# Optimization experiments

Hardware: AMD Instinct MI355X
Metric: run time of the kernel (lower is better)

The kernel has to match this reference:

```python
import jax
jax.config.update("jax_enable_x64", True)  # hashing needs true int64 like torch
import jax.numpy as jnp
import numpy as np
import itertools

N_DIM = 3
N_ENTRIES = 4194304  # 2**22
N_FEATURE = 4
BATCH = 2097152  # 2**21 sample points
GRIDS = np.array([128.0, 128.0, 128.0], dtype=np.float32)
PRIMES = np.array([1, 19349663, 83492791], dtype=np.int64)
BIT_TABLE = np.array(list(itertools.product([0, 1], repeat=N_DIM)), dtype=np.int32)  # (2^D, D)


def setup_inputs() -> dict:
    key = jax.random.key(0)
    k1, k2 = jax.random.split(key)
    position = jax.random.uniform(k1, (BATCH, N_DIM), dtype=jnp.float32)  # in [0,1)^D
    hash_table = (jax.random.uniform(k2, (N_ENTRIES, N_FEATURE), dtype=jnp.float32) - 0.5) * 2e-4
    return {"position": position, "hash_table": hash_table}


def reference(position, hash_table):
    grids = jnp.asarray(GRIDS)           # (D,) float32
    bit = jnp.asarray(BIT_TABLE)         # (2^D, D) int32
    primes = jnp.asarray(PRIMES)         # (D,) int64

    # findGrid: lower corner on the integer grid
    lower = jnp.floor(position * grids).astype(jnp.int32)          # (B, D)
    # all 2^D corners of the enclosing cell
    corner = lower[:, None, :] + bit[None, :, :]                    # (B, 2^D, D)

    # spatial hash: XOR of index*prime, reduced mod table size each step (as torch does)
    h = jnp.zeros(corner.shape[:-1], dtype=jnp.int64)               # (B, 2^D)
    for i in range(N_DIM):
        h = jnp.bitwise_xor(h, corner[..., i].astype(jnp.int64) * primes[i]) % N_ENTRIES

    corner_value = hash_table[h]                                    # (B, 2^D, F) gather

    # multilinear interpolation coefficients (faithful to source's weight assignment)
    lower_f = lower / grids                                         # (B, D)
    upper_f = (lower + 1) / grids                                   # (B, D)
    size = (upper_f - lower_f)[0]                                   # (D,) uniform cell size
    coef = jnp.stack([(position - lower_f) / size,
                      (upper_f - position) / size], axis=-1)        # (B, D, 2)
    # weight per corner = prod over dims of the bit-selected coefficient
    w = jnp.prod(coef[:, jnp.arange(N_DIM)[None, :], bit], axis=2)  # (B, 2^D)

    return jnp.sum(corner_value * w[..., None], axis=1)             # (B, F)
```

## Files before the change

### kernel.cpp

```cpp
#include <hip/hip_runtime.h>
#include <stdint.h>


#define HASH_MASK 0x3FFFFFu
#define P1 19349663u
#define P2 83492791u
#define NBUCK 64
#define CHUNKS 16
#define FB 64
#define NSUP 4096
#define PPT 16
#define K3_BLOCK 256
#define PPB (K3_BLOCK * PPT)
#define CMAX 2560

__device__ __forceinline__ uint32_t bucket_of(float px, float py, float pz) {
    uint32_t bx = ((uint32_t)(int)floorf(px * 128.0f)) >> 5;
    uint32_t by = ((uint32_t)(int)floorf(py * 128.0f)) >> 5;
    uint32_t bz = ((uint32_t)(int)floorf(pz * 128.0f)) >> 5;
    return (bx << 4) | (by << 2) | bz;
}

__device__ __forceinline__ uint32_t fine_of(float px, float py, float pz) {
    uint32_t fx = (((uint32_t)(int)floorf(px * 128.0f)) >> 3) & 3u;
    uint32_t fy = (((uint32_t)(int)floorf(py * 128.0f)) >> 3) & 3u;
    uint32_t fz = (((uint32_t)(int)floorf(pz * 128.0f)) >> 3) & 3u;
    return (fx << 4) | (fy << 2) | fz;
}

__device__ __forceinline__ float4 interp_point(float px, float py, float pz,
                                               const float* __restrict__ table) {
    int lx = (int)floorf(px * 128.0f);
    int ly = (int)floorf(py * 128.0f);
    int lz = (int)floorf(pz * 128.0f);
    const float inv = 1.0f / 128.0f;
    float w0x = (px - (float)lx * inv) * 128.0f;
    float w1x = ((float)(lx + 1) * inv - px) * 128.0f;
    float w0y = (py - (float)ly * inv) * 128.0f;
    float w1y = ((float)(ly + 1) * inv - py) * 128.0f;
    float w0z = (pz - (float)lz * inv) * 128.0f;
    float w1z = ((float)(lz + 1) * inv - pz) * 128.0f;
    uint32_t hx0 = (uint32_t)lx, hx1 = (uint32_t)(lx + 1);
    uint32_t hy0 = (uint32_t)ly * P1, hy1 = (uint32_t)(ly + 1) * P1;
    uint32_t hz0 = (uint32_t)lz * P2, hz1 = (uint32_t)(lz + 1) * P2;
    float acc0 = 0.f, acc1 = 0.f, acc2 = 0.f, acc3 = 0.f;
#pragma unroll
    for (int c = 0; c < 8; ++c) {
        int bx = (c >> 2) & 1, by = (c >> 1) & 1, bz = c & 1;
        uint32_t h = ((bx ? hx1 : hx0) ^ (by ? hy1 : hy0) ^ (bz ? hz1 : hz0)) & HASH_MASK;
        const float4 v = *reinterpret_cast<const float4*>(table + (size_t)h * 4);
        float w = ((bx ? w1x : w0x) * (by ? w1y : w0y)) * (bz ? w1z : w0z);
        acc0 += v.x * w; acc1 += v.y * w; acc2 += v.z * w; acc3 += v.w * w;
    }
    return make_float4(acc0, acc1, acc2, acc3);
}

__global__ __launch_bounds__(K3_BLOCK) void hist_kernel(
    const float* __restrict__ pos, uint32_t* __restrict__ hist, int batch)
{
    __shared__ uint32_t h[NBUCK];
    int tid = threadIdx.x;
    size_t start = (size_t)blockIdx.x * PPB;
    if (tid < NBUCK) h[tid] = 0;
    __syncthreads();
#pragma unroll
    for (int k = 0; k < PPT; ++k) {
        size_t i = start + (size_t)k * K3_BLOCK + tid;
        if (i < (size_t)batch) {
            float px = pos[3 * i + 0];
            float py = pos[3 * i + 1];
            float pz = pos[3 * i + 2];
            atomicAdd(&h[bucket_of(px, py, pz)], 1u);
        }
    }
    __syncthreads();
    if (tid < NBUCK && h[tid]) atomicAdd(&hist[tid], h[tid]);
}

__global__ __launch_bounds__(64) void scan_kernel(
    const uint32_t* __restrict__ hist, uint32_t* __restrict__ cursor)
{
    int t = threadIdx.x;
    uint32_t v = hist[t];
    uint32_t inc = v;
    for (int off = 1; off < 64; off <<= 1) {
        uint32_t n = __shfl_up(inc, off);
        if (t >= off) inc += n;
    }
    cursor[t] = inc - v;
}

__global__ __launch_bounds__(K3_BLOCK) void scatter_kernel(
    const float* __restrict__ pos, uint32_t* __restrict__ cursor,
    float4* __restrict__ sorted, int batch)
{
    __shared__ float4 staged[PPB];
    __shared__ uint32_t h[NBUCK], lbase[NBUCK], gbase[NBUCK], lcur[NBUCK];
    int tid = threadIdx.x;
    size_t start = (size_t)blockIdx.x * PPB;

    if (tid < NBUCK) h[tid] = 0;
    __syncthreads();

    float px[PPT], py[PPT], pz[PPT];
    uint32_t bb[PPT];
#pragma unroll
    for (int k = 0; k < PPT; ++k) {
        size_t i = start + (size_t)k * K3_BLOCK + tid;
        px[k] = pos[3 * i + 0];
        py[k] = pos[3 * i + 1];
        pz[k] = pos[3 * i + 2];
        bb[k] = bucket_of(px[k], py[k], pz[k]);
        atomicAdd(&h[bb[k]], 1u);
    }
    __syncthreads();

    if (tid < NBUCK) {
        uint32_t v = h[tid];
        uint32_t inc = v;
        for (int off = 1; off < 64; off <<= 1) {
            uint32_t n = __shfl_up(inc, off);
            if (tid >= off) inc += n;
        }
        uint32_t excl = inc - v;
        lbase[tid] = excl;
        lcur[tid] = excl;
        gbase[tid] = atomicAdd(&cursor[tid], v);
    }
    __syncthreads();

#pragma unroll
    for (int k = 0; k < PPT; ++k) {
        size_t i = start + (size_t)k * K3_BLOCK + tid;
        uint32_t slot = atomicAdd(&lcur[bb[k]], 1u);
        staged[slot] = make_float4(px[k], py[k], pz[k], __uint_as_float((uint32_t)i));
    }
    __syncthreads();

#pragma unroll
    for (int k = 0; k < PPT; ++k) {
        int j = k * K3_BLOCK + tid;
        float4 s = staged[j];
        uint32_t b = bucket_of(s.x, s.y, s.z);
        sorted[gbase[b] + ((uint32_t)j - lbase[b])] = s;
    }
}

__global__ __launch_bounds__(256) void fineA_kernel(
    const float4* __restrict__ sorted, const uint32_t* __restrict__ cursor,
    uint32_t* __restrict__ chist)
{
    __shared__ uint32_t h[FB];
    int tid = threadIdx.x;
    int b = blockIdx.x >> 4, c = blockIdx.x & (CHUNKS - 1);
    uint32_t bs = b ? cursor[b - 1] : 0u;
    uint32_t be = cursor[b];
    uint32_t n = be - bs;
    uint32_t csz = (n + CHUNKS - 1) / CHUNKS;
    uint32_t cs = bs + (uint32_t)c * csz;
    uint32_t ce = min(cs + csz, be);

    if (tid < FB) h[tid] = 0;
    __syncthreads();
    for (uint32_t j = cs + tid; j < ce; j += 256) {
        float4 s = sorted[j];
        atomicAdd(&h[fine_of(s.x, s.y, s.z)], 1u);
    }
    __syncthreads();
    if (tid < FB) chist[((uint32_t)blockIdx.x << 6) + tid] = h[tid];
}

__global__ __launch_bounds__(64) void fineB_kernel(
    uint32_t* __restrict__ chist, const uint32_t* __restrict__ cursor,
    uint32_t* __restrict__ sstart)
{
    int b = blockIdx.x;
    int f = threadIdx.x;
    uint32_t bs = b ? cursor[b - 1] : 0u;

    uint32_t cnt[CHUNKS];
    uint32_t tot = 0;
#pragma unroll
    for (int c = 0; c < CHUNKS; ++c) {
        cnt[c] = chist[(((uint32_t)b * CHUNKS + c) << 6) + f];
        tot += cnt[c];
    }
    uint32_t inc = tot;
    for (int off = 1; off < 64; off <<= 1) {
        uint32_t n = __shfl_up(inc, off);
        if (f >= off) inc += n;
    }
    uint32_t fbase = bs + inc - tot;
    sstart[((uint32_t)b << 6) + f] = fbase;
    uint32_t run = fbase;
#pragma unroll
    for (int c = 0; c < CHUNKS; ++c) {
        chist[(((uint32_t)b * CHUNKS + c) << 6) + f] = run;
        run += cnt[c];
    }
}

__global__ __launch_bounds__(256) void fineC_kernel(
    const float4* __restrict__ sorted, const uint32_t* __restrict__ cursor,
    const uint32_t* __restrict__ cbase, float4* __restrict__ sorted2)
{
    __shared__ float4 staged[CMAX];
    __shared__ uint32_t h[FB], lbase[FB], lcur[FB], gb[FB];
    int tid = threadIdx.x;
    int b = blockIdx.x >> 4, c = blockIdx.x & (CHUNKS - 1);
    uint32_t bs = b ? cursor[b - 1] : 0u;
    uint32_t be = cursor[b];
    uint32_t n = be - bs;
    uint32_t csz = (n + CHUNKS - 1) / CHUNKS;
    uint32_t cs = bs + (uint32_t)c * csz;
    uint32_t ce = min(cs + csz, be);
    if (ce <= cs) return;
    uint32_t m = ce - cs;

    if (tid < FB) h[tid] = 0;
    __syncthreads();

    for (uint32_t j = cs + tid; j < ce; j += 256)  {
        float4 s = sorted[j];
        atomicAdd(&h[fine_of(s.x, s.y, s.z)], 1u);
    }
    __syncthreads();

    if (tid < FB) {
        uint32_t v = h[tid];
        uint32_t inc = v;
        for (int off = 1; off < 64; off <<= 1) {
            uint32_t nn = __shfl_up(inc, off);
            if (tid >= off) inc += nn;
        }
        lbase[tid] = inc - v;
        lcur[tid] = inc - v;
        gb[tid] = cbase[(((uint32_t)b * CHUNKS + c) << 6) + tid];
    }
    __syncthreads();

    for (uint32_t j = cs + tid; j < ce; j += 256) {
        float4 s = sorted[j];
        uint32_t slot = atomicAdd(&lcur[fine_of(s.x, s.y, s.z)], 1u);
        staged[slot] = s;
    }
    __syncthreads();

    for (uint32_t j = tid; j < m; j += 256) {
        float4 s = staged[j];
        uint32_t f = fine_of(s.x, s.y, s.z);
        sorted2[gb[f] + (j - lbase[f])] = s;
    }
}

__global__ __launch_bounds__(256) void interp_super_kernel(
    const float4* __restrict__ sorted2, const uint32_t* __restrict__ sstart,
    const float* __restrict__ table, float4* __restrict__ out4, int batch)
{
    __shared__ float4 corners[729];
    int bid = blockIdx.x;
    int swz = (bid & 7) * (NSUP >> 3) + (bid >> 3);
    int tid = threadIdx.x;
    uint32_t r = (uint32_t)swz;
    uint32_t start = sstart[r];
    uint32_t end = (r == NSUP - 1) ? (uint32_t)batch : sstart[r + 1];
    if (start >= end) return;

    float4 s0 = sorted2[start];
    int rbx = (((int)floorf(s0.x * 128.0f)) >> 3) << 3;
    int rby = (((int)floorf(s0.y * 128.0f)) >> 3) << 3;
    int rbz = (((int)floorf(s0.z * 128.0f)) >> 3) << 3;

    for (int idx = tid; idx < 729; idx += 256) {
        int ci = idx / 81;
        int rem = idx - ci * 81;
        int cj = rem / 9;
        int ck = rem - cj * 9;
        uint32_t h = ((uint32_t)(rbx + ci) ^
                      (uint32_t)(rby + cj) * P1 ^
                      (uint32_t)(rbz + ck) * P2) & HASH_MASK;
        corners[idx] = *reinterpret_cast<const float4*>(table + (size_t)h * 4);
    }
    __syncthreads();

    const float inv = 1.0f / 128.0f;
    for (uint32_t p = start + tid; p < end; p += 256) {
        float4 s = sorted2[p];
        float px = s.x, py = s.y, pz = s.z;
        int lx = (int)floorf(px * 128.0f);
        int ly = (int)floorf(py * 128.0f);
        int lz = (int)floorf(pz * 128.0f);
        float w0x = (px - (float)lx * inv) * 128.0f;
        float w1x = ((float)(lx + 1) * inv - px) * 128.0f;
        float w0y = (py - (float)ly * inv) * 128.0f;
        float w1y = ((float)(ly + 1) * inv - py) * 128.0f;
        float w0z = (pz - (float)lz * inv) * 128.0f;
        float w1z = ((float)(lz + 1) * inv - pz) * 128.0f;
        int li = lx - rbx, lj = ly - rby, lk = lz - rbz;
        int base = li * 81 + lj * 9 + lk;

        float acc0 = 0.f, acc1 = 0.f, acc2 = 0.f, acc3 = 0.f;
#pragma unroll
        for (int c = 0; c < 8; ++c) {
            int bx = (c >> 2) & 1, by = (c >> 1) & 1, bz = c & 1;
            float4 v = corners[base + bx * 81 + by * 9 + bz];
            float w = ((bx ? w1x : w0x) * (by ? w1y : w0y)) * (bz ? w1z : w0z);
            acc0 += v.x * w; acc1 += v.y * w; acc2 += v.z * w; acc3 += v.w * w;
        }
        out4[__float_as_uint(s.w)] = make_float4(acc0, acc1, acc2, acc3);
    }
}

__global__ __launch_bounds__(256) void interp_scatter_kernel(
    const float4* __restrict__ sorted, const float* __restrict__ table,
    float4* __restrict__ out4, int batch, int nwg)
{
    int bid = blockIdx.x;
    int q = nwg >> 3;
    int swz = (bid & 7) * q + (bid >> 3);
    int i = swz * 256 + threadIdx.x;
    if (i >= batch) return;
    float4 s = sorted[i];
    float4 r = interp_point(s.x, s.y, s.z, table);
    out4[__float_as_uint(s.w)] = r;
}

__global__ __launch_bounds__(256) void interp_direct_kernel(
    const float* __restrict__ pos, const float* __restrict__ table,
    float4* __restrict__ out4, int batch)
{
    int i = blockIdx.x * 256 + threadIdx.x;
    if (i >= batch) return;
    out4[i] = interp_point(pos[3 * (size_t)i], pos[3 * (size_t)i + 1],
                           pos[3 * (size_t)i + 2], table);
}

extern "C" void kernel_launch(void* const* d_in, const int* in_sizes, int n_in,
                              void* d_out, int out_size, void* d_ws, size_t ws_size,
                              hipStream_t stream) {
    const float* pos   = (const float*)d_in[0];
    const float* table = (const float*)d_in[1];
    float4* out4 = (float4*)d_out;

    int batch = in_sizes[0] / 3;
    int blocks256 = (batch + 255) / 256;

    size_t sorted_off  = 512;
    size_t sorted2_off = sorted_off + (size_t)batch * 16;
    size_t chist_off   = sorted2_off + (size_t)batch * 16;
    size_t chist_bytes = (size_t)NBUCK * CHUNKS * FB * 4;
    size_t sstart_off  = chist_off + chist_bytes;
    size_t need_min  = sorted_off + (size_t)batch * 16;
    size_t need_full = sstart_off + (size_t)NSUP * 4;

    bool exact = (batch % PPB == 0) && ((blocks256 & 7) == 0);
    if (ws_size < need_min || !exact) {
        interp_direct_kernel<<<blocks256, 256, 0, stream>>>(pos, table, out4, batch);
        return;
    }

    uint32_t* hist    = (uint32_t*)d_ws;
    uint32_t* cursor  = (uint32_t*)((char*)d_ws + 256);
    float4*   sorted  = (float4*)((char*)d_ws + sorted_off);
    float4*   sorted2 = (float4*)((char*)d_ws + sorted2_off);
    uint32_t* chist   = (uint32_t*)((char*)d_ws + chist_off);
    uint32_t* sstart  = (uint32_t*)((char*)d_ws + sstart_off);

    int sblocks = batch / PPB;

    hipMemsetAsync(hist, 0, NBUCK * sizeof(uint32_t), stream);
    hist_kernel<<<sblocks, K3_BLOCK, 0, stream>>>(pos, hist, batch);
    scan_kernel<<<1, 64, 0, stream>>>(hist, cursor);
    scatter_kernel<<<sblocks, K3_BLOCK, 0, stream>>>(pos, cursor, sorted, batch);

    if (ws_size >= need_full) {
        fineA_kernel<<<NBUCK * CHUNKS, 256, 0, stream>>>(sorted, cursor, chist);
        fineB_kernel<<<NBUCK, 64, 0, stream>>>(chist, cursor, sstart);
        fineC_kernel<<<NBUCK * CHUNKS, 256, 0, stream>>>(sorted, cursor, chist, sorted2);
        interp_super_kernel<<<NSUP, 256, 0, stream>>>(sorted2, sstart, table, out4, batch);
    } else {
        interp_scatter_kernel<<<blocks256, 256, 0, stream>>>(sorted, table, out4,
                                                             batch, blocks256);
    }
}
```

Measured before the change: 110.9 us.

## Store per-point fine-bucket keys and reuse chunk histograms in fine sort

The scatter kernel now writes a one-byte fine-bucket key for each sorted point. fineA builds its histograms from these keys instead of rereading the 16-byte points. fineC no longer recomputes the per-chunk histogram with a full extra pass over sorted data; it reads the counts fineA already stored, and fineB writes the prefix bases to a separate cbase array so those counts survive. This removes roughly two full reads of the 32 MB sorted buffer at the cost of writing and reading a 2 MB key array, and it drops the fallback scatter path.

```diff
diff --git a/kernel.cpp b/kernel.cpp
--- a/kernel.cpp
+++ b/kernel.cpp
@@ -92,7 +92,7 @@
 
 __global__ __launch_bounds__(K3_BLOCK) void scatter_kernel(
     const float* __restrict__ pos, uint32_t* __restrict__ cursor,
-    float4* __restrict__ sorted, int batch)
+    float4* __restrict__ sorted, uint8_t* __restrict__ key, int batch)
 {
     __shared__ float4 staged[PPB];
     __shared__ uint32_t h[NBUCK], lbase[NBUCK], gbase[NBUCK], lcur[NBUCK];
@@ -142,12 +142,14 @@
         int j = k * K3_BLOCK + tid;
         float4 s = staged[j];
         uint32_t b = bucket_of(s.x, s.y, s.z);
-        sorted[gbase[b] + ((uint32_t)j - lbase[b])] = s;
+        uint32_t slot = gbase[b] + ((uint32_t)j - lbase[b]);
+        sorted[slot] = s;
+        key[slot] = (uint8_t)fine_of(s.x, s.y, s.z);
     }
 }
 
 __global__ __launch_bounds__(256) void fineA_kernel(
-    const float4* __restrict__ sorted, const uint32_t* __restrict__ cursor,
+    const uint8_t* __restrict__ key, const uint32_t* __restrict__ cursor,
     uint32_t* __restrict__ chist)
 {
     __shared__ uint32_t h[FB];
@@ -162,17 +164,15 @@
 
     if (tid < FB) h[tid] = 0;
     __syncthreads();
-    for (uint32_t j = cs + tid; j < ce; j += 256) {
-        float4 s = sorted[j];
-        atomicAdd(&h[fine_of(s.x, s.y, s.z)], 1u);
-    }
+    for (uint32_t j = cs + tid; j < ce; j += 256)
+        atomicAdd(&h[key[j]], 1u);
     __syncthreads();
     if (tid < FB) chist[((uint32_t)blockIdx.x << 6) + tid] = h[tid];
 }
 
 __global__ __launch_bounds__(64) void fineB_kernel(
-    uint32_t* __restrict__ chist, const uint32_t* __restrict__ cursor,
-    uint32_t* __restrict__ sstart)
+    const uint32_t* __restrict__ chist, const uint32_t* __restrict__ cursor,
+    uint32_t* __restrict__ cbase, uint32_t* __restrict__ sstart)
 {
     int b = blockIdx.x;
     int f = threadIdx.x;
@@ -195,17 +195,18 @@
     uint32_t run = fbase;
 #pragma unroll
     for (int c = 0; c < CHUNKS; ++c) {
-        chist[(((uint32_t)b * CHUNKS + c) << 6) + f] = run;
+        cbase[(((uint32_t)b * CHUNKS + c) << 6) + f] = run;
         run += cnt[c];
     }
 }
 
 __global__ __launch_bounds__(256) void fineC_kernel(
-    const float4* __restrict__ sorted, const uint32_t* __restrict__ cursor,
+    const float4* __restrict__ sorted, const uint8_t* __restrict__ key,
+    const uint32_t* __restrict__ cursor, const uint32_t* __restrict__ chist,
     const uint32_t* __restrict__ cbase, float4* __restrict__ sorted2)
 {
     __shared__ float4 staged[CMAX];
-    __shared__ uint32_t h[FB], lbase[FB], lcur[FB], gb[FB];
+    __shared__ uint32_t lbase[FB], lcur[FB], gb[FB];
     int tid = threadIdx.x;
     int b = blockIdx.x >> 4, c = blockIdx.x & (CHUNKS - 1);
     uint32_t bs = b ? cursor[b - 1] : 0u;
@@ -217,17 +218,8 @@
     if (ce <= cs) return;
     uint32_t m = ce - cs;
 
-    if (tid < FB) h[tid] = 0;
-    __syncthreads();
-
-    for (uint32_t j = cs + tid; j < ce; j += 256)  {
-        float4 s = sorted[j];
-        atomicAdd(&h[fine_of(s.x, s.y, s.z)], 1u);
-    }
-    __syncthreads();
-
     if (tid < FB) {
-        uint32_t v = h[tid];
+        uint32_t v = chist[(((uint32_t)b * CHUNKS + c) << 6) + tid];
         uint32_t inc = v;
         for (int off = 1; off < 64; off <<= 1) {
             uint32_t nn = __shfl_up(inc, off);
@@ -241,7 +233,7 @@
 
     for (uint32_t j = cs + tid; j < ce; j += 256) {
         float4 s = sorted[j];
-        uint32_t slot = atomicAdd(&lcur[fine_of(s.x, s.y, s.z)], 1u);
+        uint32_t slot = atomicAdd(&lcur[key[j]], 1u);
         staged[slot] = s;
     }
     __syncthreads();
@@ -311,20 +303,6 @@
     }
 }
 
-__global__ __launch_bounds__(256) void interp_scatter_kernel(
-    const float4* __restrict__ sorted, const float* __restrict__ table,
-    float4* __restrict__ out4, int batch, int nwg)
-{
-    int bid = blockIdx.x;
-    int q = nwg >> 3;
-    int swz = (bid & 7) * q + (bid >> 3);
-    int i = swz * 256 + threadIdx.x;
-    if (i >= batch) return;
-    float4 s = sorted[i];
-    float4 r = interp_point(s.x, s.y, s.z, table);
-    out4[__float_as_uint(s.w)] = r;
-}
-
 __global__ __launch_bounds__(256) void interp_direct_kernel(
     const float* __restrict__ pos, const float* __restrict__ table,
     float4* __restrict__ out4, int batch)
@@ -349,12 +327,13 @@
     size_t sorted2_off = sorted_off + (size_t)batch * 16;
     size_t chist_off   = sorted2_off + (size_t)batch * 16;
     size_t chist_bytes = (size_t)NBUCK * CHUNKS * FB * 4;
-    size_t sstart_off  = chist_off + chist_bytes;
-    size_t need_min  = sorted_off + (size_t)batch * 16;
-    size_t need_full = sstart_off + (size_t)NSUP * 4;
+    size_t cbase_off   = chist_off + chist_bytes;
+    size_t sstart_off  = cbase_off + chist_bytes;
+    size_t key_off     = sstart_off + (size_t)NSUP * 4;
+    size_t need_full   = key_off + (size_t)batch;
 
     bool exact = (batch % PPB == 0) && ((blocks256 & 7) == 0);
-    if (ws_size < need_min || !exact) {
+    if (ws_size < need_full || !exact) {
         interp_direct_kernel<<<blocks256, 256, 0, stream>>>(pos, table, out4, batch);
         return;
     }
@@ -364,22 +343,19 @@
     float4*   sorted  = (float4*)((char*)d_ws + sorted_off);
     float4*   sorted2 = (float4*)((char*)d_ws + sorted2_off);
     uint32_t* chist   = (uint32_t*)((char*)d_ws + chist_off);
+    uint32_t* cbase   = (uint32_t*)((char*)d_ws + cbase_off);
     uint32_t* sstart  = (uint32_t*)((char*)d_ws + sstart_off);
+    uint8_t*  key     = (uint8_t*)((char*)d_ws + key_off);
 
     int sblocks = batch / PPB;
 
     hipMemsetAsync(hist, 0, NBUCK * sizeof(uint32_t), stream);
     hist_kernel<<<sblocks, K3_BLOCK, 0, stream>>>(pos, hist, batch);
     scan_kernel<<<1, 64, 0, stream>>>(hist, cursor);
-    scatter_kernel<<<sblocks, K3_BLOCK, 0, stream>>>(pos, cursor, sorted, batch);
-
-    if (ws_size >= need_full) {
-        fineA_kernel<<<NBUCK * CHUNKS, 256, 0, stream>>>(sorted, cursor, chist);
-        fineB_kernel<<<NBUCK, 64, 0, stream>>>(chist, cursor, sstart);
-        fineC_kernel<<<NBUCK * CHUNKS, 256, 0, stream>>>(sorted, cursor, chist, sorted2);
-        interp_super_kernel<<<NSUP, 256, 0, stream>>>(sorted2, sstart, table, out4, batch);
-    } else {
-        interp_scatter_kernel<<<blocks256, 256, 0, stream>>>(sorted, table, out4,
-                                                             batch, blocks256);
-    }
-}
+    scatter_kernel<<<sblocks, K3_BLOCK, 0, stream>>>(pos, cursor, sorted, key, batch);
+    fineA_kernel<<<NBUCK * CHUNKS, 256, 0, stream>>>(key, cursor, chist);
+    fineB_kernel<<<NBUCK, 64, 0, stream>>>(chist, cursor, cbase, sstart);
+    fineC_kernel<<<NBUCK * CHUNKS, 256, 0, stream>>>(sorted, key, cursor, chist,
+                                                     cbase, sorted2);
+    interp_super_kernel<<<NSUP, 256, 0, stream>>>(sorted2, sstart, table, out4, batch);
+}
```

Measured after the change: 106.9 us. -3.6%, faster.
